# Performance work log

Hardware: AMD Instinct MI355X
Metric: run time of the kernel (lower is better)

## Reference

```python
import jax, jax.numpy as jnp
import numpy as np

T = 2048          # tokens (flattened batch*seq, vLLM style)
HID = 2048        # hidden_size
NH = 16           # num_heads
D_NOPE = 128
D_ROPE = 64
D_QK = D_NOPE + D_ROPE   # 192
D_V = 128
Q_LORA = 1536
KV_LORA = 512
THETA = 10000.0
EPS = 1e-6
SCALING = D_QK ** -0.5


def _rmsnorm(x, g):
    return x * jax.lax.rsqrt(jnp.mean(x * x, axis=-1, keepdims=True) + EPS) * g


def _rope(pos, x):
    # interleaved (is_neox_style=False) rotary embedding
    d = x.shape[-1]
    inv = 1.0 / (THETA ** (jnp.arange(0, d, 2, dtype=jnp.float32) / d))
    f = pos.astype(jnp.float32)[:, None] * inv          # [T, d/2]
    cos, sin = jnp.cos(f), jnp.sin(f)
    for _ in range(x.ndim - 2):                          # broadcast over heads
        cos, sin = cos[:, None], sin[:, None]
    x1, x2 = x[..., 0::2], x[..., 1::2]
    o1 = x1 * cos - x2 * sin
    o2 = x1 * sin + x2 * cos
    return jnp.stack([o1, o2], axis=-1).reshape(x.shape)


def setup_inputs() -> dict:
    key = jax.random.key(0)
    ks = jax.random.split(key, 6)
    s = 0.02
    return {
        "hidden_states": jax.random.normal(ks[0], (T, HID), jnp.float32),
        "positions": jnp.arange(T, dtype=jnp.int32),
        "w_qkv_a": jax.random.normal(ks[1], (HID, Q_LORA + KV_LORA + D_ROPE), jnp.float32) * s,
        "g_q": jnp.ones((Q_LORA,), jnp.float32),
        "w_q_b": jax.random.normal(ks[2], (Q_LORA, NH * D_QK), jnp.float32) * s,
        "g_kv": jnp.ones((KV_LORA,), jnp.float32),
        "w_kv_b": jax.random.normal(ks[3], (KV_LORA, NH * (D_NOPE + D_V)), jnp.float32) * s,
        "w_o": jax.random.normal(ks[4], (NH * D_V, HID), jnp.float32) * s,
    }


def reference(hidden_states, positions, w_qkv_a, g_q, w_q_b, g_kv, w_kv_b, w_o):
    # fused low-rank a-projection: [T, q_lora + kv_lora + rope]
    qkv_a = hidden_states @ w_qkv_a
    q_lat = qkv_a[:, :Q_LORA]
    kv_lat = qkv_a[:, Q_LORA:Q_LORA + KV_LORA]
    k_pe = qkv_a[:, Q_LORA + KV_LORA:]                   # [T, rope]

    # query path: rmsnorm -> b-projection -> [T, H, d_qk]
    q = (_rmsnorm(q_lat, g_q) @ w_q_b).reshape(T, NH, D_QK)
    q_nope, q_pe = q[..., :D_NOPE], q[..., D_NOPE:]

    # kv path: rmsnorm -> b-projection -> [T, H, nope + v]
    kv = (_rmsnorm(kv_lat, g_kv) @ w_kv_b).reshape(T, NH, D_NOPE + D_V)
    k_nope, v = kv[..., :D_NOPE], kv[..., D_NOPE:]

    q_pe = _rope(positions, q_pe)                        # [T, H, rope]
    k_pe = _rope(positions, k_pe)                        # [T, rope] shared MQA rope key

    qf = jnp.concatenate([q_nope, q_pe], axis=-1)        # [T, H, d_qk]
    kf = jnp.concatenate([k_nope, jnp.broadcast_to(k_pe[:, None, :], (T, NH, D_ROPE))], axis=-1)

    scores = jnp.einsum("thd,shd->hts", qf, kf) * SCALING   # [H, T, T]
    mask = jnp.tril(jnp.ones((T, T), dtype=bool))
    scores = jnp.where(mask, scores, jnp.finfo(scores.dtype).min)
    probs = jax.nn.softmax(scores, axis=-1)
    out = jnp.einsum("hts,shd->thd", probs, v)           # [T, H, d_v]
    return out.reshape(T, NH * D_V) @ w_o                # [T, hidden]
```

## Files before the change

### kernel.cpp

```cpp
#include <hip/hip_runtime.h>
#include <hip/hip_bf16.h>
#include <math.h>

typedef __bf16 bf16_t;
typedef __bf16 bf16x8 __attribute__((ext_vector_type(8)));
typedef float floatx4 __attribute__((ext_vector_type(4)));
typedef int intx4 __attribute__((ext_vector_type(4)));

#define T_TOK 2048
#define HID 2048
#define NH 16
#define D_NOPE 128
#define D_ROPE 64
#define D_QK 192
#define D_V 128
#define Q_LORA 1536
#define KV_LORA 512
#define QKV_N 2112
#define QKV_NPAD 2176
#define SCALING 0.07216878364870323f
#define LOG2E 1.442695041f
#define EXP_C1 (SCALING * LOG2E)
#define EXP_C2 (12.0f * LOG2E)

#define MFMA_BF16(a, b, c) __builtin_amdgcn_mfma_f32_16x16x32_bf16(a, b, c, 0, 0, 0)

__device__ __forceinline__ void gload16(const void* g, void* l) {
    __builtin_amdgcn_global_load_lds(
        (const __attribute__((address_space(1))) unsigned int*)g,
        (__attribute__((address_space(3))) unsigned int*)l, 16, 0, 0);
}

template <int MODE>
__global__ __launch_bounds__(256) void gemm_mfma(
    const bf16_t* __restrict__ A, const bf16_t* __restrict__ Bt,
    float* __restrict__ Cf, bf16_t* __restrict__ Cb,
    bf16_t* __restrict__ kfull, bf16_t* __restrict__ vtmp,
    int M, int N, int K)
{
    __shared__ __align__(16) bf16_t As[2][2 * 128 * 32];
    __shared__ __align__(16) bf16_t Bs[2][2 * 128 * 32];
    const int tid = threadIdx.x;
    const int lane = tid & 63;
    const int w = tid >> 6;
    const int wm = w >> 1, wn = w & 1;
    const int m0 = blockIdx.y * 128, n0 = blockIdx.x * 128;
    const int l15 = lane & 15, quad = lane >> 4;

    floatx4 acc[4][4] = {};

#define GSTAGE(db_, k0_)                                                                 \
    do {                                                                                 \
        _Pragma("unroll")                                                                \
        for (int it = 0; it < 4; ++it) {                                                 \
            int slot = it * 256 + tid;                                                   \
            int kk2 = slot >> 9;                                                         \
            int r = (slot >> 2) & 127;                                                   \
            int c = slot & 3;                                                            \
            gload16((const char*)(A + (size_t)(m0 + r) * K + (k0_) + kk2 * 32 + c * 8),  \
                    (char*)As[db_] + slot * 16);                                         \
            gload16((const char*)(Bt + (size_t)(n0 + r) * K + (k0_) + kk2 * 32 + c * 8), \
                    (char*)Bs[db_] + slot * 16);                                         \
        }                                                                                \
    } while (0)

    GSTAGE(0, 0);
    int db = 0;
    for (int k0 = 0; k0 < K; k0 += 64) {
        __syncthreads();
        if (k0 + 64 < K) GSTAGE(db ^ 1, k0 + 64);
#pragma unroll
        for (int kk2 = 0; kk2 < 2; ++kk2) {
            bf16x8 af[4], bfr[4];
#pragma unroll
            for (int mi = 0; mi < 4; ++mi)
                af[mi] = *(const bf16x8*)(As[db] + kk2 * 4096 +
                                          (wm * 64 + mi * 16 + l15) * 32 + quad * 8);
#pragma unroll
            for (int ni = 0; ni < 4; ++ni)
                bfr[ni] = *(const bf16x8*)(Bs[db] + kk2 * 4096 +
                                           (wn * 64 + ni * 16 + l15) * 32 + quad * 8);
#pragma unroll
            for (int mi = 0; mi < 4; ++mi)
#pragma unroll
                for (int ni = 0; ni < 4; ++ni)
                    acc[mi][ni] = MFMA_BF16(af[mi], bfr[ni], acc[mi][ni]);
        }
        db ^= 1;
    }
#undef GSTAGE

#pragma unroll
    for (int mi = 0; mi < 4; ++mi)
#pragma unroll
        for (int ni = 0; ni < 4; ++ni)
#pragma unroll
            for (int r = 0; r < 4; ++r) {
                int row = m0 + wm * 64 + mi * 16 + quad * 4 + r;
                int col = n0 + wn * 64 + ni * 16 + l15;
                float v = acc[mi][ni][r];
                if (MODE == 0) {
                    Cf[(size_t)row * N + col] = v;
                } else if (MODE == 1) {
                    Cb[(size_t)row * N + col] = (bf16_t)v;
                } else {
                    int h = col >> 8, dd = col & 255;
                    if (dd < 128)
                        kfull[((size_t)h * T_TOK + row) * 192 + dd] = (bf16_t)v;
                    else
                        vtmp[(size_t)row * 2048 + h * 128 + (dd - 128)] = (bf16_t)v;
                }
            }
}

__global__ void transpose_all(const float* __restrict__ w0, const float* __restrict__ w1,
                              const float* __restrict__ w2, const float* __restrict__ w3,
                              bf16_t* __restrict__ o0, bf16_t* __restrict__ o1,
                              bf16_t* __restrict__ o2, bf16_t* __restrict__ o3) {
    const float* in; bf16_t* out; int K, N;
    switch (blockIdx.z) {
        case 0: in = w0; out = o0; K = 2048; N = 2112; break;
        case 1: in = w1; out = o1; K = 1536; N = 3072; break;
        case 2: in = w2; out = o2; K = 512;  N = 4096; break;
        default: in = w3; out = o3; K = 2048; N = 2048; break;
    }
    int n0 = blockIdx.x * 32, k0 = blockIdx.y * 32;
    if (n0 >= N || k0 >= K) return;
    __shared__ float tile[32][33];
    int tx = threadIdx.x, ty = threadIdx.y;
    for (int i = ty; i < 32; i += 8)
        tile[i][tx] = in[(size_t)(k0 + i) * N + n0 + tx];
    __syncthreads();
    for (int i = ty; i < 32; i += 8)
        out[(size_t)(n0 + i) * K + k0 + tx] = (bf16_t)tile[tx][i];
}

__global__ void transpose_b2b(const bf16_t* __restrict__ in, bf16_t* __restrict__ out,
                              int R, int C) {
    __shared__ bf16_t tile[32][33];
    int c0 = blockIdx.x * 32, r0 = blockIdx.y * 32;
    int tx = threadIdx.x, ty = threadIdx.y;
    for (int i = ty; i < 32; i += 8)
        tile[i][tx] = in[(size_t)(r0 + i) * C + c0 + tx];
    __syncthreads();
    for (int i = ty; i < 32; i += 8)
        out[(size_t)(c0 + i) * R + r0 + tx] = tile[tx][i];
}

__global__ void cvt_f2b(const float* __restrict__ in, bf16_t* __restrict__ out, int n) {
    int i = blockIdx.x * 256 + threadIdx.x;
    if (i < n) out[i] = (bf16_t)in[i];
}

__global__ void mid_fuse(const float* __restrict__ qkv_a, const int* __restrict__ pos,
                         const float* __restrict__ g_q, const float* __restrict__ g_kv,
                         bf16_t* __restrict__ qn, bf16_t* __restrict__ kvn,
                         bf16_t* __restrict__ kfull) {
    int t = blockIdx.x, tid = threadIdx.x;
    const float* x = qkv_a + (size_t)t * QKV_NPAD;
    __shared__ float red[256];
    float ss = 0.f;
    for (int c = tid; c < Q_LORA; c += 256) { float v = x[c]; ss += v * v; }
    red[tid] = ss;
    __syncthreads();
    for (int o = 128; o > 0; o >>= 1) {
        if (tid < o) red[tid] += red[tid + o];
        __syncthreads();
    }
    float rq = rsqrtf(red[0] / (float)Q_LORA + 1e-6f);
    __syncthreads();
    ss = 0.f;
    for (int c = Q_LORA + tid; c < Q_LORA + KV_LORA; c += 256) { float v = x[c]; ss += v * v; }
    red[tid] = ss;
    __syncthreads();
    for (int o = 128; o > 0; o >>= 1) {
        if (tid < o) red[tid] += red[tid + o];
        __syncthreads();
    }
    float rkv = rsqrtf(red[0] / (float)KV_LORA + 1e-6f);

    for (int c = tid; c < Q_LORA; c += 256)
        qn[(size_t)t * Q_LORA + c] = (bf16_t)(x[c] * rq * g_q[c]);
    for (int c = tid; c < KV_LORA; c += 256)
        kvn[(size_t)t * KV_LORA + c] = (bf16_t)(x[Q_LORA + c] * rkv * g_kv[c]);

    if (tid < 32) {
        int i = tid;
        double inv = pow(10000.0, -(double)(2 * i) / 64.0);
        double fd = (double)pos[t] * inv;
        float c = (float)cos(fd), s = (float)sin(fd);
        float x1 = x[Q_LORA + KV_LORA + 2 * i], x2 = x[Q_LORA + KV_LORA + 2 * i + 1];
        bf16_t v0 = (bf16_t)(x1 * c - x2 * s);
        bf16_t v1 = (bf16_t)(x1 * s + x2 * c);
#pragma unroll
        for (int h = 0; h < NH; ++h) {
            kfull[((size_t)h * T_TOK + t) * 192 + 128 + 2 * i] = v0;
            kfull[((size_t)h * T_TOK + t) * 192 + 128 + 2 * i + 1] = v1;
        }
    }
}

__global__ void rope_q_kernel(bf16_t* __restrict__ q, const int* __restrict__ pos) {
    int idx = blockIdx.x * blockDim.x + threadIdx.x;
    if (idx >= T_TOK * NH * 32) return;
    int i = idx & 31;
    int h = (idx >> 5) & (NH - 1);
    int t = idx >> 9;
    double inv = pow(10000.0, -(double)(2 * i) / 64.0);
    double fd = (double)pos[t] * inv;
    float c = (float)cos(fd), s = (float)sin(fd);
    bf16_t* base = q + (size_t)t * (NH * D_QK) + h * D_QK + D_NOPE;
    float x1 = (float)base[2 * i], x2 = (float)base[2 * i + 1];
    base[2 * i] = (bf16_t)(x1 * c - x2 * s);
    base[2 * i + 1] = (bf16_t)(x1 * s + x2 * c);
}

__global__ __launch_bounds__(256, 2) void attn_part(
    const bf16_t* __restrict__ qbuf, const bf16_t* __restrict__ kfull,
    const bf16_t* __restrict__ vT,
    bf16_t* __restrict__ oP0, bf16_t* __restrict__ oP1, float* __restrict__ l_part)
{
    const int id = blockIdx.x;
    const int h = id & 15;
    const int c = (id >> 4) & 3;
    const int qt = 15 - (id >> 6);
    const int q0 = qt * 128;
    const int nTile = 2 * (qt + 1);
    const int tbase = nTile >> 2, trem = nTile & 3;
    const int sz = tbase + (c < trem ? 1 : 0);
    const int sBeg = c * tbase + (c < trem ? c : trem);
    const int sEnd = sBeg + sz;
    const int unit = qt * 16 + h;
    const int tid = threadIdx.x, lane = tid & 63, w = tid >> 6;
    const int l15 = lane & 15, quad = lane >> 4;
    const int ckey = (l15 >> 1) & 3;

    __shared__ __align__(16) bf16_t kn2[2][6 * 64 * 32];
    __shared__ __align__(16) bf16_t vt2[2 * 128 * 32];
    __shared__ __align__(16) bf16_t p_s[128 * 64];

    bf16x8 qf[2][6];
#pragma unroll
    for (int st = 0; st < 2; ++st) {
        const bf16_t* qp = qbuf + (size_t)(q0 + w * 32 + st * 16 + l15) * (NH * D_QK) +
                           h * D_QK;
#pragma unroll
        for (int kk = 0; kk < 6; ++kk)
            qf[st][kk] = *(const bf16x8*)(qp + kk * 32 + quad * 8);
    }

    bf16x8 ones;
#pragma unroll
    for (int j = 0; j < 8; ++j) ones[j] = (bf16_t)1.0f;

    floatx4 o[2][8] = {};
    floatx4 lac[2] = {};
    intx4 vreg[4];

#define STAGE_KN(buf_, s0_)                                                              \
    do {                                                                                 \
        _Pragma("unroll")                                                                \
        for (int it = 0; it < 6; ++it) {                                                 \
            int slot = it * 256 + tid;                                                   \
            int kk = slot >> 8, s = (slot >> 2) & 63, cc = slot & 3;                     \
            int cs = cc ^ ((s >> 1) & 3);                                                \
            gload16((const char*)(kfull + ((size_t)h * T_TOK + (s0_) + s) * 192 +        \
                                  kk * 32 + cs * 8),                                     \
                    (char*)kn2[buf_] + slot * 16);                                       \
        }                                                                                \
    } while (0)

#define VLOAD(s0_)                                                                       \
    do {                                                                                 \
        _Pragma("unroll")                                                                \
        for (int it = 0; it < 4; ++it) {                                                 \
            int slot = it * 256 + tid;                                                   \
            int ks = slot >> 9, d = (slot >> 2) & 127, cc = slot & 3;                    \
            vreg[it] = *(const intx4*)(vT + ((size_t)h * 128 + d) * T_TOK + (s0_) +      \
                                       ks * 32 + cc * 8);                                \
        }                                                                                \
    } while (0)

#define VWRITE()                                                                         \
    do {                                                                                 \
        _Pragma("unroll")                                                                \
        for (int it = 0; it < 4; ++it) {                                                 \
            int slot = it * 256 + tid;                                                   \
            int ks = slot >> 9, d = (slot >> 2) & 127, cc = slot & 3;                    \
            *(intx4*)((char*)vt2 +                                                       \
                      (size_t)((ks * 512 + d * 4 + (cc ^ ((d >> 1) & 3))) * 16)) =       \
                vreg[it];                                                                \
        }                                                                                \
    } while (0)

    if (sz > 0) {
        VLOAD(sBeg * 64);
        STAGE_KN(0, sBeg * 64);
        VWRITE();
    }

    for (int si = sBeg; si < sEnd; ++si) {
        const int s0 = si * 64;
        const int buf = (si - sBeg) & 1;
        __syncthreads();
        if (si + 1 < sEnd) {
            VLOAD(s0 + 64);
            STAGE_KN(buf ^ 1, s0 + 64);
        }

        floatx4 s_acc[2][4] = {};
        __builtin_amdgcn_s_setprio(1);
#pragma unroll
        for (int ni = 0; ni < 4; ++ni) {
#pragma unroll
            for (int kk = 0; kk < 6; ++kk) {
                bf16x8 b = *(const bf16x8*)(kn2[buf] + kk * 2048 +
                                            (ni * 16 + l15) * 32 + (quad ^ ckey) * 8);
                s_acc[0][ni] = MFMA_BF16(qf[0][kk], b, s_acc[0][ni]);
                s_acc[1][ni] = MFMA_BF16(qf[1][kk], b, s_acc[1][ni]);
            }
        }
        __builtin_amdgcn_s_setprio(0);

        const bool diag = (si >= 2 * qt);
#pragma unroll
        for (int st = 0; st < 2; ++st)
#pragma unroll
            for (int ni = 0; ni < 4; ++ni)
#pragma unroll
                for (int r = 0; r < 4; ++r) {
                    int prow = w * 32 + st * 16 + quad * 4 + r;
                    int pcol = ni * 16 + l15;
                    float pv = exp2f(s_acc[st][ni][r] * EXP_C1 - EXP_C2);
                    if (diag && (s0 + pcol) > (q0 + prow)) pv = 0.f;
                    p_s[prow * 64 + ((((pcol >> 3) ^ (prow & 7))) << 3) + (pcol & 7)] =
                        (bf16_t)pv;
                }

        __builtin_amdgcn_s_setprio(1);
#pragma unroll
        for (int ks = 0; ks < 2; ++ks) {
            bf16x8 a0, a1;
            {
                int arow = w * 32 + l15;
                a0 = *(const bf16x8*)(p_s + arow * 64 +
                                      (((ks * 4 + quad) ^ (arow & 7)) << 3));
                arow += 16;
                a1 = *(const bf16x8*)(p_s + arow * 64 +
                                      (((ks * 4 + quad) ^ (arow & 7)) << 3));
            }
            lac[0] = MFMA_BF16(a0, ones, lac[0]);
            lac[1] = MFMA_BF16(a1, ones, lac[1]);
#pragma unroll
            for (int ni = 0; ni < 8; ++ni) {
                bf16x8 b = *(const bf16x8*)(vt2 + ks * 4096 +
                                            (ni * 16 + l15) * 32 + (quad ^ ckey) * 8);
                o[0][ni] = MFMA_BF16(a0, b, o[0][ni]);
                o[1][ni] = MFMA_BF16(a1, b, o[1][ni]);
            }
        }
        __builtin_amdgcn_s_setprio(0);

        __syncthreads();
        if (si + 1 < sEnd) VWRITE();
    }

    bf16_t* op = ((c < 2) ? oP0 : oP1) + (size_t)(unit * 2 + (c & 1)) * 128 * 128;
#pragma unroll
    for (int st = 0; st < 2; ++st) {
#pragma unroll
        for (int ni = 0; ni < 8; ++ni)
#pragma unroll
            for (int r = 0; r < 4; ++r) {
                int lrow = w * 32 + st * 16 + quad * 4 + r;
                op[(size_t)lrow * 128 + ni * 16 + l15] = (bf16_t)o[st][ni][r];
            }
        if (l15 == 0)
#pragma unroll
            for (int r = 0; r < 4; ++r) {
                int lrow = w * 32 + st * 16 + quad * 4 + r;
                l_part[((size_t)unit * 4 + c) * 128 + lrow] = lac[st][r];
            }
    }
#undef STAGE_KN
#undef VLOAD
#undef VWRITE
}

__global__ void attn_combine(const bf16_t* __restrict__ oP0,
                             const bf16_t* __restrict__ oP1,
                             const float* __restrict__ l_part,
                             bf16_t* __restrict__ attn_o)
{
    int idx = blockIdx.x * 256 + threadIdx.x;
    int t = idx >> 8, cg = idx & 255;
    int col = cg * 8;
    int h = col >> 7, d = col & 127;
    int qt = t >> 7, lrow = t & 127;
    size_t unit = (size_t)qt * 16 + h;
    const float* lp = l_part + unit * 4 * 128 + lrow;
    float inv = 1.f / (lp[0] + lp[128] + lp[256] + lp[384]);
    size_t r0 = ((unit * 2 + 0) * 128 + lrow) * 128 + d;
    size_t r1 = ((unit * 2 + 1) * 128 + lrow) * 128 + d;
    bf16x8 a0 = *(const bf16x8*)(oP0 + r0);
    bf16x8 a1 = *(const bf16x8*)(oP0 + r1);
    bf16x8 a2 = *(const bf16x8*)(oP1 + r0);
    bf16x8 a3 = *(const bf16x8*)(oP1 + r1);
    bf16x8 out;
#pragma unroll
    for (int j = 0; j < 8; ++j)
        out[j] = (bf16_t)(((float)a0[j] + (float)a1[j] + (float)a2[j] + (float)a3[j]) * inv);
    *(bf16x8*)(attn_o + (size_t)t * (NH * D_V) + col) = out;
}

extern "C" void kernel_launch(void* const* d_in, const int* in_sizes, int n_in,
                              void* d_out, int out_size, void* d_ws, size_t ws_size,
                              hipStream_t stream) {
    const float* hidden = (const float*)d_in[0];
    const int* positions = (const int*)d_in[1];
    const float* w_qkv_a = (const float*)d_in[2];
    const float* g_q = (const float*)d_in[3];
    const float* w_q_b = (const float*)d_in[4];
    const float* g_kv = (const float*)d_in[5];
    const float* w_kv_b = (const float*)d_in[6];
    const float* w_o = (const float*)d_in[7];
    float* out = (float*)d_out;

    char* p = (char*)d_ws;
    float* qkv_a = (float*)p;
    bf16_t* attn_o = (bf16_t*)p;
    p += (size_t)T_TOK * QKV_NPAD * 4;
    bf16_t* hbf = (bf16_t*)p;
    bf16_t* qn = hbf;
    bf16_t* kvn = hbf + (size_t)T_TOK * Q_LORA;
    p += (size_t)T_TOK * HID * 2;
    bf16_t* qbuf = (bf16_t*)p;  p += (size_t)T_TOK * NH * D_QK * 2;
    bf16_t* vtmp = (bf16_t*)p;  p += (size_t)T_TOK * NH * D_V * 2;
    bf16_t* kfull = (bf16_t*)p; p += (size_t)NH * T_TOK * 192 * 2;
    bf16_t* vT = (bf16_t*)p;    p += (size_t)NH * 128 * T_TOK * 2;
    bf16_t* wt_qkv_a = (bf16_t*)p; p += (size_t)QKV_NPAD * HID * 2;
    bf16_t* wt_q_b = (bf16_t*)p;   p += (size_t)3072 * Q_LORA * 2;
    bf16_t* wt_kv_b = (bf16_t*)p;  p += (size_t)4096 * KV_LORA * 2;
    bf16_t* wt_o = (bf16_t*)p;

    bf16_t* oP0 = wt_qkv_a;
    bf16_t* oP1 = (bf16_t*)((char*)d_ws + (size_t)T_TOK * HID * 2);
    float* l_part = (float*)vtmp;

    dim3 tb(32, 8);

    cvt_f2b<<<(T_TOK * HID) / 256, 256, 0, stream>>>(hidden, hbf, T_TOK * HID);
    transpose_all<<<dim3(128, 64, 4), tb, 0, stream>>>(
        w_qkv_a, w_q_b, w_kv_b, w_o, wt_qkv_a, wt_q_b, wt_kv_b, wt_o);

    gemm_mfma<0><<<dim3(QKV_NPAD / 128, T_TOK / 128), 256, 0, stream>>>(
        hbf, wt_qkv_a, qkv_a, nullptr, nullptr, nullptr, T_TOK, QKV_NPAD, HID);

    mid_fuse<<<T_TOK, 256, 0, stream>>>(qkv_a, positions, g_q, g_kv, qn, kvn, kfull);

    gemm_mfma<1><<<dim3(3072 / 128, T_TOK / 128), 256, 0, stream>>>(
        qn, wt_q_b, nullptr, qbuf, nullptr, nullptr, T_TOK, 3072, Q_LORA);
    rope_q_kernel<<<(T_TOK * NH * 32) / 256, 256, 0, stream>>>(qbuf, positions);

    gemm_mfma<2><<<dim3(4096 / 128, T_TOK / 128), 256, 0, stream>>>(
        kvn, wt_kv_b, nullptr, nullptr, kfull, vtmp, T_TOK, 4096, KV_LORA);
    transpose_b2b<<<dim3(HID / 32, T_TOK / 32), tb, 0, stream>>>(vtmp, vT, T_TOK, HID);

    attn_part<<<1024, 256, 0, stream>>>(qbuf, kfull, vT, oP0, oP1, l_part);
    attn_combine<<<(T_TOK * 256) / 256, 256, 0, stream>>>(oP0, oP1, l_part, attn_o);

    gemm_mfma<0><<<dim3(HID / 128, T_TOK / 128), 256, 0, stream>>>(
        attn_o, wt_o, out, nullptr, nullptr, nullptr, T_TOK, HID, NH * D_V);
}
```

Baseline: 349.6 us.

## Merge q/kv b-projection GEMMs into one launch; load attention K/V straight to registers

The two b-projection GEMMs become a single dual-purpose kernel, removing one launch and letting both GEMMs share the GPU. Separately, the attention kernel drops its double-buffered LDS staging of K and V (and the block barriers) and reads K and V fragments directly from global memory into registers for the MFMAs. This frees LDS and barrier cost, and the launch-bounds occupancy hint of 2 is removed. The price is uncoalesced, duplicated global reads per wave, since each of the four waves now fetches the same K/V tiles on its own, plus higher register pressure from holding 16 V fragments.

New measurement: 402.1 us. +15.0%, slower.

```diff
diff --git a/kernel.cpp b/kernel.cpp
--- a/kernel.cpp
+++ b/kernel.cpp
@@ -32,19 +32,16 @@
 }
 
 template <int MODE>
-__global__ __launch_bounds__(256) void gemm_mfma(
+__device__ __forceinline__ void gemm_body(
     const bf16_t* __restrict__ A, const bf16_t* __restrict__ Bt,
     float* __restrict__ Cf, bf16_t* __restrict__ Cb,
     bf16_t* __restrict__ kfull, bf16_t* __restrict__ vtmp,
-    int M, int N, int K)
+    int N, int K, int m0, int n0, bf16_t* As, bf16_t* Bs)
 {
-    __shared__ __align__(16) bf16_t As[2][2 * 128 * 32];
-    __shared__ __align__(16) bf16_t Bs[2][2 * 128 * 32];
     const int tid = threadIdx.x;
     const int lane = tid & 63;
     const int w = tid >> 6;
     const int wm = w >> 1, wn = w & 1;
-    const int m0 = blockIdx.y * 128, n0 = blockIdx.x * 128;
     const int l15 = lane & 15, quad = lane >> 4;
 
     floatx4 acc[4][4] = {};
@@ -58,9 +55,9 @@
             int r = (slot >> 2) & 127;                                                   \
             int c = slot & 3;                                                            \
             gload16((const char*)(A + (size_t)(m0 + r) * K + (k0_) + kk2 * 32 + c * 8),  \
-                    (char*)As[db_] + slot * 16);                                         \
+                    (char*)(As + (db_)*8192) + slot * 16);                               \
             gload16((const char*)(Bt + (size_t)(n0 + r) * K + (k0_) + kk2 * 32 + c * 8), \
-                    (char*)Bs[db_] + slot * 16);                                         \
+                    (char*)(Bs + (db_)*8192) + slot * 16);                               \
         }                                                                                \
     } while (0)
 
@@ -74,11 +71,11 @@
             bf16x8 af[4], bfr[4];
 #pragma unroll
             for (int mi = 0; mi < 4; ++mi)
-                af[mi] = *(const bf16x8*)(As[db] + kk2 * 4096 +
+                af[mi] = *(const bf16x8*)(As + db * 8192 + kk2 * 4096 +
                                           (wm * 64 + mi * 16 + l15) * 32 + quad * 8);
 #pragma unroll
             for (int ni = 0; ni < 4; ++ni)
-                bfr[ni] = *(const bf16x8*)(Bs[db] + kk2 * 4096 +
+                bfr[ni] = *(const bf16x8*)(Bs + db * 8192 + kk2 * 4096 +
                                            (wn * 64 + ni * 16 + l15) * 32 + quad * 8);
 #pragma unroll
             for (int mi = 0; mi < 4; ++mi)
@@ -113,6 +110,38 @@
             }
 }
 
+template <int MODE>
+__global__ __launch_bounds__(256) void gemm_mfma(
+    const bf16_t* __restrict__ A, const bf16_t* __restrict__ Bt,
+    float* __restrict__ Cf, bf16_t* __restrict__ Cb,
+    bf16_t* __restrict__ kfull, bf16_t* __restrict__ vtmp,
+    int M, int N, int K)
+{
+    __shared__ __align__(16) bf16_t As[2 * 8192];
+    __shared__ __align__(16) bf16_t Bs[2 * 8192];
+    gemm_body<MODE>(A, Bt, Cf, Cb, kfull, vtmp, N, K,
+                    blockIdx.y * 128, blockIdx.x * 128, As, Bs);
+}
+
+__global__ __launch_bounds__(256) void gemm_dual(
+    const bf16_t* __restrict__ qn, const bf16_t* __restrict__ wqb,
+    bf16_t* __restrict__ qbuf,
+    const bf16_t* __restrict__ kvn, const bf16_t* __restrict__ wkvb,
+    bf16_t* __restrict__ kfull, bf16_t* __restrict__ vtmp)
+{
+    __shared__ __align__(16) bf16_t As[2 * 8192];
+    __shared__ __align__(16) bf16_t Bs[2 * 8192];
+    int id = blockIdx.x;
+    if (id < 384) {
+        gemm_body<1>(qn, wqb, nullptr, qbuf, nullptr, nullptr,
+                     3072, Q_LORA, (id / 24) * 128, (id % 24) * 128, As, Bs);
+    } else {
+        int i2 = id - 384;
+        gemm_body<2>(kvn, wkvb, nullptr, nullptr, kfull, vtmp,
+                     4096, KV_LORA, (i2 / 32) * 128, (i2 % 32) * 128, As, Bs);
+    }
+}
+
 __global__ void transpose_all(const float* __restrict__ w0, const float* __restrict__ w1,
                               const float* __restrict__ w2, const float* __restrict__ w3,
                               bf16_t* __restrict__ o0, bf16_t* __restrict__ o1,
@@ -215,7 +244,7 @@
     base[2 * i + 1] = (bf16_t)(x1 * s + x2 * c);
 }
 
-__global__ __launch_bounds__(256, 2) void attn_part(
+__global__ __launch_bounds__(256) void attn_part(
     const bf16_t* __restrict__ qbuf, const bf16_t* __restrict__ kfull,
     const bf16_t* __restrict__ vT,
     bf16_t* __restrict__ oP0, bf16_t* __restrict__ oP1, float* __restrict__ l_part)
@@ -233,10 +262,7 @@
     const int unit = qt * 16 + h;
     const int tid = threadIdx.x, lane = tid & 63, w = tid >> 6;
     const int l15 = lane & 15, quad = lane >> 4;
-    const int ckey = (l15 >> 1) & 3;
-
-    __shared__ __align__(16) bf16_t kn2[2][6 * 64 * 32];
-    __shared__ __align__(16) bf16_t vt2[2 * 128 * 32];
+
     __shared__ __align__(16) bf16_t p_s[128 * 64];
 
     bf16x8 qf[2][6];
@@ -255,72 +281,38 @@
 
     floatx4 o[2][8] = {};
     floatx4 lac[2] = {};
-    intx4 vreg[4];
-
-#define STAGE_KN(buf_, s0_)                                                              \
-    do {                                                                                 \
-        _Pragma("unroll")                                                                \
-        for (int it = 0; it < 6; ++it) {                                                 \
-            int slot = it * 256 + tid;                                                   \
-            int kk = slot >> 8, s = (slot >> 2) & 63, cc = slot & 3;                     \
-            int cs = cc ^ ((s >> 1) & 3);                                                \
-            gload16((const char*)(kfull + ((size_t)h * T_TOK + (s0_) + s) * 192 +        \
-                                  kk * 32 + cs * 8),                                     \
-                    (char*)kn2[buf_] + slot * 16);                                       \
-        }                                                                                \
-    } while (0)
-
-#define VLOAD(s0_)                                                                       \
-    do {                                                                                 \
-        _Pragma("unroll")                                                                \
-        for (int it = 0; it < 4; ++it) {                                                 \
-            int slot = it * 256 + tid;                                                   \
-            int ks = slot >> 9, d = (slot >> 2) & 127, cc = slot & 3;                    \
-            vreg[it] = *(const intx4*)(vT + ((size_t)h * 128 + d) * T_TOK + (s0_) +      \
-                                       ks * 32 + cc * 8);                                \
-        }                                                                                \
-    } while (0)
-
-#define VWRITE()                                                                         \
-    do {                                                                                 \
-        _Pragma("unroll")                                                                \
-        for (int it = 0; it < 4; ++it) {                                                 \
-            int slot = it * 256 + tid;                                                   \
-            int ks = slot >> 9, d = (slot >> 2) & 127, cc = slot & 3;                    \
-            *(intx4*)((char*)vt2 +                                                       \
-                      (size_t)((ks * 512 + d * 4 + (cc ^ ((d >> 1) & 3))) * 16)) =       \
-                vreg[it];                                                                \
-        }                                                                                \
-    } while (0)
-
-    if (sz > 0) {
-        VLOAD(sBeg * 64);
-        STAGE_KN(0, sBeg * 64);
-        VWRITE();
-    }
+
+    const bf16_t* krow = kfull + ((size_t)h * T_TOK) * 192 + l15 * 192 + quad * 8;
+    const bf16_t* vrow = vT + (size_t)h * 128 * T_TOK + (size_t)l15 * T_TOK + quad * 8;
 
     for (int si = sBeg; si < sEnd; ++si) {
         const int s0 = si * 64;
-        const int buf = (si - sBeg) & 1;
-        __syncthreads();
-        if (si + 1 < sEnd) {
-            VLOAD(s0 + 64);
-            STAGE_KN(buf ^ 1, s0 + 64);
-        }
-
+
+        const bf16_t* kb = krow + (size_t)s0 * 192;
         floatx4 s_acc[2][4] = {};
         __builtin_amdgcn_s_setprio(1);
 #pragma unroll
         for (int ni = 0; ni < 4; ++ni) {
+            bf16x8 bk[6];
+#pragma unroll
+            for (int kk = 0; kk < 6; ++kk)
+                bk[kk] = *(const bf16x8*)(kb + ni * (16 * 192) + kk * 32);
 #pragma unroll
             for (int kk = 0; kk < 6; ++kk) {
-                bf16x8 b = *(const bf16x8*)(kn2[buf] + kk * 2048 +
-                                            (ni * 16 + l15) * 32 + (quad ^ ckey) * 8);
-                s_acc[0][ni] = MFMA_BF16(qf[0][kk], b, s_acc[0][ni]);
-                s_acc[1][ni] = MFMA_BF16(qf[1][kk], b, s_acc[1][ni]);
+                s_acc[0][ni] = MFMA_BF16(qf[0][kk], bk[kk], s_acc[0][ni]);
+                s_acc[1][ni] = MFMA_BF16(qf[1][kk], bk[kk], s_acc[1][ni]);
             }
         }
         __builtin_amdgcn_s_setprio(0);
+
+        bf16x8 bv[16];
+        const bf16_t* vb = vrow + s0;
+#pragma unroll
+        for (int ks = 0; ks < 2; ++ks)
+#pragma unroll
+            for (int ni = 0; ni < 8; ++ni)
+                bv[ks * 8 + ni] =
+                    *(const bf16x8*)(vb + (size_t)ni * (16 * T_TOK) + ks * 32);
 
         const bool diag = (si >= 2 * qt);
 #pragma unroll
@@ -353,16 +345,11 @@
             lac[1] = MFMA_BF16(a1, ones, lac[1]);
 #pragma unroll
             for (int ni = 0; ni < 8; ++ni) {
-                bf16x8 b = *(const bf16x8*)(vt2 + ks * 4096 +
-                                            (ni * 16 + l15) * 32 + (quad ^ ckey) * 8);
-                o[0][ni] = MFMA_BF16(a0, b, o[0][ni]);
-                o[1][ni] = MFMA_BF16(a1, b, o[1][ni]);
+                o[0][ni] = MFMA_BF16(a0, bv[ks * 8 + ni], o[0][ni]);
+                o[1][ni] = MFMA_BF16(a1, bv[ks * 8 + ni], o[1][ni]);
             }
         }
         __builtin_amdgcn_s_setprio(0);
-
-        __syncthreads();
-        if (si + 1 < sEnd) VWRITE();
     }
 
     bf16_t* op = ((c < 2) ? oP0 : oP1) + (size_t)(unit * 2 + (c & 1)) * 128 * 128;
@@ -382,9 +369,6 @@
                 l_part[((size_t)unit * 4 + c) * 128 + lrow] = lac[st][r];
             }
     }
-#undef STAGE_KN
-#undef VLOAD
-#undef VWRITE
 }
 
 __global__ void attn_combine(const bf16_t* __restrict__ oP0,
@@ -458,12 +442,8 @@
 
     mid_fuse<<<T_TOK, 256, 0, stream>>>(qkv_a, positions, g_q, g_kv, qn, kvn, kfull);
 
-    gemm_mfma<1><<<dim3(3072 / 128, T_TOK / 128), 256, 0, stream>>>(
-        qn, wt_q_b, nullptr, qbuf, nullptr, nullptr, T_TOK, 3072, Q_LORA);
+    gemm_dual<<<896, 256, 0, stream>>>(qn, wt_q_b, qbuf, kvn, wt_kv_b, kfull, vtmp);
     rope_q_kernel<<<(T_TOK * NH * 32) / 256, 256, 0, stream>>>(qbuf, positions);
-
-    gemm_mfma<2><<<dim3(4096 / 128, T_TOK / 128), 256, 0, stream>>>(
-        kvn, wt_kv_b, nullptr, nullptr, kfull, vtmp, T_TOK, 4096, KV_LORA);
     transpose_b2b<<<dim3(HID / 32, T_TOK / 32), tb, 0, stream>>>(vtmp, vT, T_TOK, HID);
 
     attn_part<<<1024, 256, 0, stream>>>(qbuf, kfull, vT, oP0, oP1, l_part);
```
